# Performance work log

Measured on AMD Instinct MI355X. Metric: run time of the kernel, lower is better.

Reference implementation:

```python
import jax, jax.numpy as jnp
import numpy as np

MAX_KLEN = 11  # kernel lengths drawn from {7, 9, 11}


def setup_inputs() -> dict:
    B, T, K = 32, 512, 4096
    rng = np.random.default_rng(0)
    # kernel lengths ~ uniform over {7, 9, 11}
    klen = np.array([7, 9, 11])[rng.integers(0, 3, size=K)]
    tap_mask = (np.arange(MAX_KLEN)[None, :] < klen[:, None])
    # weights: N(0,1), mean-centered over the actual taps, zero-padded to MAX_KLEN
    w = rng.standard_normal((K, MAX_KLEN)).astype(np.float32) * tap_mask
    w = w - (w.sum(1, keepdims=True) / klen[:, None]).astype(np.float32) * tap_mask
    # bias ~ U[-1, 1)
    bias = (rng.random(K) * 2 - 1).astype(np.float32)
    # dilation = floor(2**s), s ~ U[0, ln(T-1) - ln(klen-1)]
    A = np.log(T - 1) - np.log(klen - 1)
    dil = np.floor(2.0 ** (rng.random(K) * A)).astype(np.int64)
    # padding = dil*(klen-1)/2 with prob 1/2, else 0  (klen-1 is even -> exact)
    pad = (dil * (klen - 1) // 2) * rng.integers(0, 2, size=K)
    # torch conv1d output length
    out_len = T + 2 * pad - dil * (klen - 1)
    x = jax.random.normal(jax.random.key(0), (B, T), dtype=jnp.float32)
    return {
        'x': x,
        'weight': jnp.asarray(w),
        'bias': jnp.asarray(bias),
        'dilation': jnp.asarray(dil, jnp.int32),
        'padding': jnp.asarray(pad, jnp.int32),
        'out_len': jnp.asarray(out_len, jnp.int32),
    }


def reference(x, weight, bias, dilation, padding, out_len):
    # x: [B, T]; weight: [K, MAX_KLEN] zero-padded; bias/dilation/padding/out_len: [K]
    B, T = x.shape
    K = weight.shape[0]
    P = T  # padding <= dil*(klen-1)/2  =>  out_len <= T
    p = jnp.arange(P, dtype=jnp.int32)
    acc = jnp.zeros((B, K, P), dtype=x.dtype)
    # fixed small loop over taps; all kernels processed at once per tap
    for j in range(MAX_KLEN):
        idx = p[None, :] - padding[:, None] + j * dilation[:, None]  # [K, P]
        ok = (idx >= 0) & (idx < T)
        xg = x[:, jnp.clip(idx, 0, T - 1)]  # [B, K, P]
        acc = acc + (weight[:, j][:, None] * ok.astype(x.dtype)) * xg
    conv = acc + bias[None, :, None]  # [B, K, P]
    valid = (p[None, :] < out_len[:, None])  # [K, P]
    neg_inf = jnp.asarray(-jnp.inf, dtype=x.dtype)
    mx = jnp.max(jnp.where(valid[None], conv, neg_inf), axis=-1)  # [B, K]
    ppv = jnp.sum(((conv > 0) & valid[None]).astype(x.dtype), axis=-1) / out_len.astype(x.dtype)
    # einops 'b s f -> b (s f)': interleave (max_k, ppv_k) per kernel
    feats = jnp.stack([mx, ppv], axis=-1).reshape(B, 2 * K)
    return feats
```

## Files before the change

kernel.cpp:

```cpp
#include <hip/hip_runtime.h>
#include <hip/hip_fp16.h>

#define TLEN 512
#define KLEN 11
#define XPAD 256
#define XTOT 1024
#define NEGINF2 0xFC00FC00u

__device__ __forceinline__ unsigned pkmax_u(unsigned a, unsigned b) {
    unsigned d;
    asm("v_pk_max_f16 %0, %1, %2" : "=v"(d) : "v"(a), "v"(b));
    return d;
}
__device__ __forceinline__ unsigned pkadd_u(unsigned a, unsigned b) {
    unsigned d;
    asm("v_pk_add_f16 %0, %1, %2" : "=v"(d) : "v"(a), "v"(b));
    return d;
}

__device__ __forceinline__ unsigned wred_pkmax(unsigned x) {
    unsigned t;
    t = __builtin_amdgcn_update_dpp((int)NEGINF2, (int)x, 0x111, 0xF, 0xF, false);
    x = pkmax_u(x, t);
    t = __builtin_amdgcn_update_dpp((int)NEGINF2, (int)x, 0x112, 0xF, 0xF, false);
    x = pkmax_u(x, t);
    t = __builtin_amdgcn_update_dpp((int)NEGINF2, (int)x, 0x114, 0xF, 0xF, false);
    x = pkmax_u(x, t);
    t = __builtin_amdgcn_update_dpp((int)NEGINF2, (int)x, 0x118, 0xF, 0xF, false);
    x = pkmax_u(x, t);
    t = __builtin_amdgcn_update_dpp((int)NEGINF2, (int)x, 0x142, 0xA, 0xF, false);
    x = pkmax_u(x, t);
    t = __builtin_amdgcn_update_dpp((int)NEGINF2, (int)x, 0x143, 0xC, 0xF, false);
    x = pkmax_u(x, t);
    return (unsigned)__builtin_amdgcn_readlane((int)x, 63);
}
__device__ __forceinline__ unsigned wred_pkadd(unsigned x) {
    unsigned t;
    t = __builtin_amdgcn_update_dpp(0, (int)x, 0x111, 0xF, 0xF, false);
    x = pkadd_u(x, t);
    t = __builtin_amdgcn_update_dpp(0, (int)x, 0x112, 0xF, 0xF, false);
    x = pkadd_u(x, t);
    t = __builtin_amdgcn_update_dpp(0, (int)x, 0x114, 0xF, 0xF, false);
    x = pkadd_u(x, t);
    t = __builtin_amdgcn_update_dpp(0, (int)x, 0x118, 0xF, 0xF, false);
    x = pkadd_u(x, t);
    t = __builtin_amdgcn_update_dpp(0, (int)x, 0x142, 0xA, 0xF, false);
    x = pkadd_u(x, t);
    t = __builtin_amdgcn_update_dpp(0, (int)x, 0x143, 0xC, 0xF, false);
    x = pkadd_u(x, t);
    return (unsigned)__builtin_amdgcn_readlane((int)x, 63);
}

__device__ __forceinline__ __half2 as_h2(unsigned u) {
    __half2 h; __builtin_memcpy(&h, &u, 4); return h;
}
__device__ __forceinline__ unsigned as_u(__half2 h) {
    unsigned u; __builtin_memcpy(&u, &h, 4); return u;
}

__global__ __launch_bounds__(256) void stage_ws_h(const float* __restrict__ x,
                                                  uint4* __restrict__ ws) {
    const int t = threadIdx.x;
    const int g = blockIdx.x >> 2;
    const int seg = blockIdx.x & 3;
    const int slot = seg * 256 + t;
    uint4 v = make_uint4(0u, 0u, 0u, 0u);
    if (slot >= XPAD && slot < XPAD + TLEN) {
        const int pos = slot - XPAD;
        const float* xg = x + (size_t)g * 8 * TLEN;
        unsigned h[8];
        #pragma unroll
        for (int q = 0; q < 8; ++q)
            h[q] = (unsigned)__half_as_ushort(__float2half(xg[q * TLEN + pos]));
        v.x = h[0] | (h[1] << 16);
        v.y = h[2] | (h[3] << 16);
        v.z = h[4] | (h[5] << 16);
        v.w = h[6] | (h[7] << 16);
    }
    ws[(size_t)g * XTOT + slot] = v;
}

__global__ __launch_bounds__(256, 4) void rf_kernel_h3(
    const uint4* __restrict__ ws, const float* __restrict__ weight,
    const float* __restrict__ bias, const int* __restrict__ dilation,
    const int* __restrict__ padding, const int* __restrict__ out_len,
    float* __restrict__ out, int K)
{
    __shared__ uint4 xs[XTOT];
    const int t = threadIdx.x;
    const uint4* wsg = ws + (size_t)blockIdx.y * XTOT;

    xs[t]       = wsg[t];
    xs[t + 256] = wsg[t + 256];
    xs[t + 512] = wsg[t + 512];
    xs[t + 768] = wsg[t + 768];
    __syncthreads();

    const int lane = t & 63;
    const int ks = __builtin_amdgcn_readfirstlane(blockIdx.x * 4 + (t >> 6));

    const int dil  = dilation[ks];
    const int pd   = padding[ks];
    const int olen = out_len[ks];
    float wjf[KLEN];
    __half2 w2[KLEN];
    #pragma unroll
    for (int j = 0; j < KLEN; ++j) {
        wjf[j] = weight[ks * KLEN + j];
        w2[j] = __float2half2_rn(wjf[j]);
    }
    const __half2 bias2 = __float2half2_rn(bias[ks]);
    const __half2 zero2 = __float2half2_rn(0.0f);

    const int vbase = XPAD + lane - pd;

    __half2 acc[8][4];
    #pragma unroll
    for (int c = 0; c < 8; ++c)
        #pragma unroll
        for (int q = 0; q < 4; ++q) acc[c][q] = bias2;

    #pragma unroll
    for (int j = 0; j < KLEN; ++j) {
        if (wjf[j] != 0.0f) {
            const uint4* xp = xs + (vbase + j * dil);
            #pragma unroll
            for (int c = 0; c < 8; ++c) {
                if (c * 64 < olen) {
                    const uint4 r = xp[c * 64];
                    acc[c][0] = __hfma2(w2[j], as_h2(r.x), acc[c][0]);
                    acc[c][1] = __hfma2(w2[j], as_h2(r.y), acc[c][1]);
                    acc[c][2] = __hfma2(w2[j], as_h2(r.z), acc[c][2]);
                    acc[c][3] = __hfma2(w2[j], as_h2(r.w), acc[c][3]);
                }
            }
        }
    }

    unsigned mxu[4], cfu[4];
    #pragma unroll
    for (int q = 0; q < 4; ++q) { mxu[q] = NEGINF2; cfu[q] = 0u; }

    #pragma unroll
    for (int c = 0; c < 8; ++c) {
        const int p0 = c * 64;
        if (p0 + 64 <= olen) {
            #pragma unroll
            for (int q = 0; q < 4; ++q) {
                mxu[q] = pkmax_u(mxu[q], as_u(acc[c][q]));
                cfu[q] = pkadd_u(cfu[q], as_u(__hgt2(acc[c][q], zero2)));
            }
        } else if (p0 < olen) {
            const bool vld = lane < (olen - p0);
            #pragma unroll
            for (int q = 0; q < 4; ++q) {
                const unsigned a = vld ? as_u(acc[c][q]) : NEGINF2;
                mxu[q] = pkmax_u(mxu[q], a);
                const unsigned g = vld ? as_u(__hgt2(acc[c][q], zero2)) : 0u;
                cfu[q] = pkadd_u(cfu[q], g);
            }
        }
    }

    #pragma unroll
    for (int q = 0; q < 4; ++q) {
        mxu[q] = wred_pkmax(mxu[q]);
        cfu[q] = wred_pkadd(cfu[q]);
    }

    if (lane == 0) {
        const float inv = 1.0f / (float)olen;
        const size_t row = (size_t)2 * K;
        float* o = out + (size_t)blockIdx.y * 8 * row + 2 * ks;
        #pragma unroll
        for (int q = 0; q < 4; ++q) {
            const __half2 m = as_h2(mxu[q]);
            const __half2 c = as_h2(cfu[q]);
            *(float2*)(o + (2 * q) * row)     = make_float2(__low2float(m),  __low2float(c) * inv);
            *(float2*)(o + (2 * q + 1) * row) = make_float2(__high2float(m), __high2float(c) * inv);
        }
    }
}

extern "C" void kernel_launch(void* const* d_in, const int* in_sizes, int n_in,
                              void* d_out, int out_size, void* d_ws, size_t ws_size,
                              hipStream_t stream) {
    const float* x    = (const float*)d_in[0];
    const float* w    = (const float*)d_in[1];
    const float* bias = (const float*)d_in[2];
    const int* dil    = (const int*)d_in[3];
    const int* pad    = (const int*)d_in[4];
    const int* olen   = (const int*)d_in[5];
    float* out        = (float*)d_out;

    const int K = in_sizes[2];
    const int B = in_sizes[0] / TLEN;
    const int G = B / 8;

    uint4* ws = (uint4*)d_ws;
    stage_ws_h<<<dim3(G * 4), 256, 0, stream>>>(x, ws);
    dim3 grid(K / 4, G);
    rf_kernel_h3<<<grid, 256, 0, stream>>>(ws, w, bias, dil, pad, olen, out, K);
    (void)n_in; (void)out_size; (void)ws_size;
}
```

Measured before the change: 90.04 us.

## Fuse fp16 staging into main kernel and use scalar-operand packed FMA

Removes the separate staging kernel: each block now loads its 8 batch rows of x directly, converts them to packed half, and writes them into LDS with zeroed padding. Weights and bias are moved to scalar registers via readfirstlane, and the FMA is issued as inline v_pk_fma_f16 with an SGPR weight operand. Launch bounds are raised to 8 blocks per SM. This saves a kernel launch and the workspace round-trip, and eases VGPR pressure. In exchange, every block redoes the fp32-to-half conversion of its x rows (K/4 times per batch group), and the higher occupancy target may cause spills.

New measurement: 90.78 us. No clear change (+0.8%).

```diff
diff --git a/kernel.cpp b/kernel.cpp
--- a/kernel.cpp
+++ b/kernel.cpp
@@ -16,6 +16,9 @@
     unsigned d;
     asm("v_pk_add_f16 %0, %1, %2" : "=v"(d) : "v"(a), "v"(b));
     return d;
+}
+__device__ __forceinline__ void pkfma_s(unsigned& acc, unsigned w2s, unsigned h) {
+    asm("v_pk_fma_f16 %0, %1, %2, %0" : "+v"(acc) : "s"(w2s), "v"(h));
 }
 
 __device__ __forceinline__ unsigned wred_pkmax(unsigned x) {
@@ -58,42 +61,32 @@
     unsigned u; __builtin_memcpy(&u, &h, 4); return u;
 }
 
-__global__ __launch_bounds__(256) void stage_ws_h(const float* __restrict__ x,
-                                                  uint4* __restrict__ ws) {
-    const int t = threadIdx.x;
-    const int g = blockIdx.x >> 2;
-    const int seg = blockIdx.x & 3;
-    const int slot = seg * 256 + t;
-    uint4 v = make_uint4(0u, 0u, 0u, 0u);
-    if (slot >= XPAD && slot < XPAD + TLEN) {
-        const int pos = slot - XPAD;
-        const float* xg = x + (size_t)g * 8 * TLEN;
-        unsigned h[8];
-        #pragma unroll
-        for (int q = 0; q < 8; ++q)
-            h[q] = (unsigned)__half_as_ushort(__float2half(xg[q * TLEN + pos]));
-        v.x = h[0] | (h[1] << 16);
-        v.y = h[2] | (h[3] << 16);
-        v.z = h[4] | (h[5] << 16);
-        v.w = h[6] | (h[7] << 16);
-    }
-    ws[(size_t)g * XTOT + slot] = v;
-}
-
-__global__ __launch_bounds__(256, 4) void rf_kernel_h3(
-    const uint4* __restrict__ ws, const float* __restrict__ weight,
+__global__ __launch_bounds__(256, 8) void rf_fused(
+    const float* __restrict__ x, const float* __restrict__ weight,
     const float* __restrict__ bias, const int* __restrict__ dilation,
     const int* __restrict__ padding, const int* __restrict__ out_len,
     float* __restrict__ out, int K)
 {
     __shared__ uint4 xs[XTOT];
     const int t = threadIdx.x;
-    const uint4* wsg = ws + (size_t)blockIdx.y * XTOT;
 
-    xs[t]       = wsg[t];
-    xs[t + 256] = wsg[t + 256];
-    xs[t + 512] = wsg[t + 512];
-    xs[t + 768] = wsg[t + 768];
+    const uint4 z = make_uint4(0u, 0u, 0u, 0u);
+    xs[t] = z;
+    xs[768 + t] = z;
+    const float* xg = x + (size_t)blockIdx.y * 8 * TLEN;
+    #pragma unroll
+    for (int half_ = 0; half_ < 2; ++half_) {
+        const int pos = t + half_ * 256;
+        float v[8];
+        #pragma unroll
+        for (int q = 0; q < 8; ++q) v[q] = xg[q * TLEN + pos];
+        uint4 s;
+        s.x = as_u(__floats2half2_rn(v[0], v[1]));
+        s.y = as_u(__floats2half2_rn(v[2], v[3]));
+        s.z = as_u(__floats2half2_rn(v[4], v[5]));
+        s.w = as_u(__floats2half2_rn(v[6], v[7]));
+        xs[XPAD + pos] = s;
+    }
     __syncthreads();
 
     const int lane = t & 63;
@@ -102,19 +95,21 @@
     const int dil  = dilation[ks];
     const int pd   = padding[ks];
     const int olen = out_len[ks];
-    float wjf[KLEN];
-    __half2 w2[KLEN];
+    unsigned w2s[KLEN];
+    bool wnz[KLEN];
     #pragma unroll
     for (int j = 0; j < KLEN; ++j) {
-        wjf[j] = weight[ks * KLEN + j];
-        w2[j] = __float2half2_rn(wjf[j]);
+        const float wv = weight[ks * KLEN + j];
+        wnz[j] = (wv != 0.0f);
+        w2s[j] = __builtin_amdgcn_readfirstlane((int)as_u(__float2half2_rn(wv)));
     }
-    const __half2 bias2 = __float2half2_rn(bias[ks]);
+    const unsigned bias2 = __builtin_amdgcn_readfirstlane(
+        (int)as_u(__float2half2_rn(bias[ks])));
     const __half2 zero2 = __float2half2_rn(0.0f);
 
     const int vbase = XPAD + lane - pd;
 
-    __half2 acc[8][4];
+    unsigned acc[8][4];
     #pragma unroll
     for (int c = 0; c < 8; ++c)
         #pragma unroll
@@ -122,16 +117,16 @@
 
     #pragma unroll
     for (int j = 0; j < KLEN; ++j) {
-        if (wjf[j] != 0.0f) {
+        if (wnz[j]) {
             const uint4* xp = xs + (vbase + j * dil);
             #pragma unroll
             for (int c = 0; c < 8; ++c) {
                 if (c * 64 < olen) {
                     const uint4 r = xp[c * 64];
-                    acc[c][0] = __hfma2(w2[j], as_h2(r.x), acc[c][0]);
-                    acc[c][1] = __hfma2(w2[j], as_h2(r.y), acc[c][1]);
-                    acc[c][2] = __hfma2(w2[j], as_h2(r.z), acc[c][2]);
-                    acc[c][3] = __hfma2(w2[j], as_h2(r.w), acc[c][3]);
+                    pkfma_s(acc[c][0], w2s[j], r.x);
+                    pkfma_s(acc[c][1], w2s[j], r.y);
+                    pkfma_s(acc[c][2], w2s[j], r.z);
+                    pkfma_s(acc[c][3], w2s[j], r.w);
                 }
             }
         }
@@ -147,16 +142,15 @@
         if (p0 + 64 <= olen) {
             #pragma unroll
             for (int q = 0; q < 4; ++q) {
-                mxu[q] = pkmax_u(mxu[q], as_u(acc[c][q]));
-                cfu[q] = pkadd_u(cfu[q], as_u(__hgt2(acc[c][q], zero2)));
+                mxu[q] = pkmax_u(mxu[q], acc[c][q]);
+                cfu[q] = pkadd_u(cfu[q], as_u(__hgt2(as_h2(acc[c][q]), zero2)));
             }
         } else if (p0 < olen) {
             const bool vld = lane < (olen - p0);
             #pragma unroll
             for (int q = 0; q < 4; ++q) {
-                const unsigned a = vld ? as_u(acc[c][q]) : NEGINF2;
-                mxu[q] = pkmax_u(mxu[q], a);
-                const unsigned g = vld ? as_u(__hgt2(acc[c][q], zero2)) : 0u;
+                mxu[q] = pkmax_u(mxu[q], vld ? acc[c][q] : NEGINF2);
+                const unsigned g = vld ? as_u(__hgt2(as_h2(acc[c][q]), zero2)) : 0u;
                 cfu[q] = pkadd_u(cfu[q], g);
             }
         }
@@ -195,11 +189,8 @@
 
     const int K = in_sizes[2];
     const int B = in_sizes[0] / TLEN;
-    const int G = B / 8;
 
-    uint4* ws = (uint4*)d_ws;
-    stage_ws_h<<<dim3(G * 4), 256, 0, stream>>>(x, ws);
-    dim3 grid(K / 4, G);
-    rf_kernel_h3<<<grid, 256, 0, stream>>>(ws, w, bias, dil, pad, olen, out, K);
-    (void)n_in; (void)out_size; (void)ws_size;
+    dim3 grid(K / 4, B / 8);
+    rf_fused<<<grid, 256, 0, stream>>>(x, w, bias, dil, pad, olen, out, K);
+    (void)n_in; (void)out_size; (void)d_ws; (void)ws_size;
 }
```
